# Kernel tuning notes

Hardware: AMD Instinct MI355X
Metric: run time of the kernel (lower is better)

Reference implementation:

```python
import jax, jax.numpy as jnp
import numpy as np

# task -> non-background class ids, padded with -1 to fixed width 3
NBG = np.array([[0, 1, 2], [0, 3, 4], [0, 5, 6], [0, 7, 8],
                [0, 9, -1], [0, 10, -1], [0, 11, -1]], dtype=np.int32)
NEG = -1e9      # pad logit (finite stand-in for -inf, grad-safe)
SMOOTH = 1e-5
NUM_CLASSES = 12


def setup_inputs() -> dict:
    key = jax.random.key(0)
    k1, k2, k3 = jax.random.split(key, 3)
    B, C, D, H, W = 4, 12, 32, 128, 128
    inputs = jax.random.normal(k1, (B, C, D, H, W), dtype=jnp.float32)
    task_id = jax.random.randint(k2, (B,), 0, 7, dtype=jnp.int32)
    # build targets consistent with each sample's task: labels in task_nbg[task]
    raw = jax.random.randint(k3, (B, D, H, W), 0, 3, dtype=jnp.int32)
    nbg = jnp.asarray(NBG)
    ids = nbg[task_id]                                   # [B,3]
    valid_max = jnp.where(ids[:, 2] < 0, 1, 2)           # 2-class tasks: raw in {0,1}
    raw = jnp.minimum(raw, valid_max[:, None, None, None])
    targets = jnp.take_along_axis(ids, raw.reshape(B, -1), axis=1).reshape(B, D, H, W)
    return {"inputs": inputs, "targets": targets, "task_id": task_id}


def reference(inputs, targets, task_id):
    B = inputs.shape[0]
    probs = jax.nn.softmax(inputs, axis=1)               # [B,12,D,H,W]
    nbg = jnp.asarray(NBG)
    ids = nbg[task_id]                                   # [B,3]
    mask = (ids >= 0)                                    # [B,3]
    idsc = jnp.maximum(ids, 0)
    mask5 = mask[:, :, None, None, None]
    gathered = jnp.take_along_axis(probs, idsc[:, :, None, None, None], axis=1)  # [B,3,D,H,W]
    score = jnp.where(mask5, gathered, 0.0)

    # --- remapped marginal targets: labels > 0 shifted by delta ---
    t = task_id.astype(jnp.int32)
    delta = jnp.where(t <= 4, -2 * t, -t - 4)
    tm = jnp.where(targets > 0, targets + delta[:, None, None, None], targets)   # in {0,1,2}

    # --- marginal CE: log_softmax over gathered probs (note: probs, not logits, matching torch F.cross_entropy on softmaxed inputs) ---
    logits = jnp.where(mask5, gathered, NEG)
    logp = jax.nn.log_softmax(logits, axis=1)
    nll = -jnp.take_along_axis(logp, tm[:, None], axis=1)[:, 0]                  # [B,D,H,W]
    loss_marg_ce = nll.mean(axis=(1, 2, 3)).sum() / B

    # --- marginal dice (padded classes contribute exactly 0) ---
    tgt = ((targets[:, None] == idsc[:, :, None, None, None]) & mask5).astype(probs.dtype)
    inter = jnp.sum(score * tgt, axis=(2, 3, 4))
    y_sum = jnp.sum(tgt, axis=(2, 3, 4))                 # tgt is binary: tgt*tgt == tgt
    z_sum = jnp.sum(score * score, axis=(2, 3, 4))
    dice = (2 * inter + SMOOTH) / (z_sum + y_sum + SMOOTH)
    loss_marg_dice = (1.0 - dice).sum() / B

    # --- exclusion: target_e = 1 - onehot(targets, 0..11), class 0 zeroed ---
    cls = jnp.arange(NUM_CLASSES, dtype=targets.dtype)[None, :, None, None, None]
    onehot = (targets[:, None] == cls).astype(probs.dtype)
    te = 1.0 - onehot
    te = te.at[:, 0].set(0.0)
    inter_e = jnp.sum(probs * te, axis=(2, 3, 4))
    y_e = jnp.sum(te, axis=(2, 3, 4))
    z_e = jnp.sum(probs * probs, axis=(2, 3, 4))
    dice_e = (2 * inter_e + SMOOTH) / (z_e + y_e + SMOOTH)
    loss_exc_dice = dice_e.sum() / B                     # inv=True: sum of dice scores

    loss_exc_ce = (jnp.log1p(probs) * te).mean(axis=(2, 3, 4)).sum() / B

    return (loss_marg_dice, loss_marg_ce, loss_exc_dice, loss_exc_ce)
```

## Files before the change

### kernel.cpp

```cpp
#include <hip/hip_runtime.h>


#define S4 131072
#define BLOCKS_PER_B 256
#define THREADS 256
#define NVOX 524288.0f
#define SMOOTH 1e-5f

#define WRED(v) { v += __shfl_down(v,32); v += __shfl_down(v,16); \
                  v += __shfl_down(v,8);  v += __shfl_down(v,4);  \
                  v += __shfl_down(v,2);  v += __shfl_down(v,1); }

#define PROC(COMP) do {                                                        \
  float xv[12];                                                                \
  _Pragma("unroll")                                                            \
  for (int c = 0; c < 12; ++c) xv[c] = x[c].COMP;                              \
  const int tgt = tg.COMP;                                                     \
  float m = xv[0];                                                             \
  _Pragma("unroll")                                                            \
  for (int c = 1; c < 12; ++c) m = fmaxf(m, xv[c]);                            \
  float e[12]; float es = 0.f;                                                 \
  _Pragma("unroll")                                                            \
  for (int c = 0; c < 12; ++c) { e[c] = __expf(xv[c] - m); es += e[c]; }       \
  const float r = __builtin_amdgcn_rcpf(es);                                   \
  float p[12];                                                                 \
  _Pragma("unroll")                                                            \
  for (int c = 0; c < 12; ++c) {                                               \
    p[c] = e[c] * r;                                                           \
    aZ[c] += p[c] * p[c];                                                      \
    aP[c] += p[c];                                                             \
  }                                                                            \
  float slog = 0.f;                                                            \
  _Pragma("unroll")                                                            \
  for (int c = 1; c < 12; ++c) slog += __logf(1.f + p[c]);                     \
  const float g0 = p[0];                                                       \
  float g1 = 0.f, g2 = 0.f;                                                    \
  _Pragma("unroll")                                                            \
  for (int c = 1; c < 12; ++c) {                                               \
    if (c==1||c==3||c==5||c==7||c==9||c==10||c==11) g1 = (id1==c) ? p[c] : g1; \
    else                                            g2 = (id2==c) ? p[c] : g2; \
  }                                                                            \
  const bool t0 = (tgt == 0);                                                  \
  const bool t1 = (tgt == id1);                                                \
  const bool t2 = v2 && (tgt == id2);                                          \
  c0 += t0 ? 1.f : 0.f;  c1 += t1 ? 1.f : 0.f;  c2 += t2 ? 1.f : 0.f;          \
  p0S += t0 ? g0 : 0.f;  p1S += t1 ? g1 : 0.f;  p2S += t2 ? g2 : 0.f;          \
  const float pt = t1 ? g1 : (t2 ? g2 : 0.f);                                  \
  cesE += slog - __logf(1.f + pt);                                             \
  float m3 = fmaxf(g0, g1);                                                    \
  if (v2) m3 = fmaxf(m3, g2);                                                  \
  float s3 = __expf(g0 - m3) + __expf(g1 - m3);                                \
  if (v2) s3 += __expf(g2 - m3);                                               \
  const float lse = m3 + __logf(s3);                                           \
  const float gt = t0 ? g0 : (t1 ? g1 : g2);                                   \
  ces += lse - gt;                                                             \
} while (0)

__global__ void zero_acc(float* __restrict__ acc) {
  acc[threadIdx.x] = 0.f;
}

__global__ __launch_bounds__(THREADS, 4)
void marg_main(const float4* __restrict__ inp, const int4* __restrict__ tgtp,
               const int* __restrict__ task_id, float* __restrict__ acc) {
  const int b   = blockIdx.x / BLOCKS_PER_B;
  const int blk = blockIdx.x % BLOCKS_PER_B;
  const int t   = task_id[b];
  const int id1 = (t <= 4) ? 2*t + 1 : t + 5;
  const int id2 = (t <= 3) ? 2*t + 2 : -1;
  const bool v2 = (id2 >= 0);

  const float4* inB = inp  + (size_t)b * 12 * S4;
  const int4*   tgB = tgtp + (size_t)b * S4;

  float aZ[12], aP[12];
  #pragma unroll
  for (int c = 0; c < 12; ++c) { aZ[c]=0.f; aP[c]=0.f; }
  float ces=0.f, cesE=0.f, c0=0.f, c1=0.f, c2=0.f, p0S=0.f, p1S=0.f, p2S=0.f;

  #pragma unroll 1
  for (int it = 0; it < 2; ++it) {
    const int s = (blk * 2 + it) * THREADS + (int)threadIdx.x;
    float4 x[12];
    #pragma unroll
    for (int c = 0; c < 12; ++c) x[c] = inB[c * S4 + s];
    const int4 tg = tgB[s];
    PROC(x); PROC(y); PROC(z); PROC(w);
  }

  WRED(ces); WRED(cesE); WRED(c0); WRED(c1); WRED(c2);
  WRED(p0S); WRED(p1S); WRED(p2S);
  #pragma unroll
  for (int c = 0; c < 12; ++c) { WRED(aZ[c]); WRED(aP[c]); }

  __shared__ float red[4][32];
  const int lane = threadIdx.x & 63;
  const int wv   = threadIdx.x >> 6;
  if (lane == 0) {
    float* rw = red[wv];
    rw[0]=ces; rw[1]=cesE; rw[2]=c0; rw[3]=c1; rw[4]=c2;
    rw[5]=p0S; rw[6]=p1S; rw[7]=p2S;
    #pragma unroll
    for (int c = 0; c < 12; ++c) { rw[8+c]=aZ[c]; rw[20+c]=aP[c]; }
  }
  __syncthreads();
  if (threadIdx.x < 32) {
    const float sv = red[0][threadIdx.x] + red[1][threadIdx.x]
                   + red[2][threadIdx.x] + red[3][threadIdx.x];
    atomicAdd(acc + b * 64 + threadIdx.x, sv);
  }
}

__global__ void finalize(const float* __restrict__ acc,
                         const int* __restrict__ task_id,
                         float* __restrict__ out) {
  if (threadIdx.x != 0) return;
  float lmd = 0.f, lmce = 0.f, led = 0.f, lece = 0.f;
  for (int b = 0; b < 4; ++b) {
    const float* a = acc + b * 64;
    const int t   = task_id[b];
    const int id1 = (t <= 4) ? 2*t + 1 : t + 5;
    const int id2 = (t <= 3) ? 2*t + 2 : -1;

    lmce += a[0] / NVOX;
    lece += a[1] / NVOX;

    const float d0 = (2.f*a[5] + SMOOTH) / (a[8 + 0]   + a[2] + SMOOTH);
    const float d1 = (2.f*a[6] + SMOOTH) / (a[8 + id1] + a[3] + SMOOTH);
    float d2 = 1.f;
    if (id2 >= 0)
      d2 = (2.f*a[7] + SMOOTH) / (a[8 + id2] + a[4] + SMOOTH);
    lmd += (1.f - d0) + (1.f - d1) + (1.f - d2);

    led += SMOOTH / (a[8] + SMOOTH);
    for (int c = 1; c < 12; ++c) {
      const float ptc  = (c == id1) ? a[6] : ((c == id2) ? a[7] : 0.f);
      const float cntc = (c == id1) ? a[3] : ((c == id2) ? a[4] : 0.f);
      const float inter = a[20 + c] - ptc;
      const float ye    = NVOX - cntc;
      led += (2.f*inter + SMOOTH) / (a[8 + c] + ye + SMOOTH);
    }
  }
  out[0] = lmd  * 0.25f;
  out[1] = lmce * 0.25f;
  out[2] = led  * 0.25f;
  out[3] = lece * 0.25f;
}

extern "C" void kernel_launch(void* const* d_in, const int* in_sizes, int n_in,
                              void* d_out, int out_size, void* d_ws, size_t ws_size,
                              hipStream_t stream) {
  const float* inputs  = (const float*)d_in[0];
  const int*   targets = (const int*)d_in[1];
  const int*   task_id = (const int*)d_in[2];
  float* out = (float*)d_out;
  float* acc = (float*)d_ws;

  zero_acc<<<1, 256, 0, stream>>>(acc);
  marg_main<<<dim3(4 * BLOCKS_PER_B), THREADS, 0, stream>>>(
      (const float4*)inputs, (const int4*)targets, task_id, acc);
  finalize<<<1, 64, 0, stream>>>(acc, task_id, out);
}
```

Measured before the change: 167.2 us.

## Cut transcendental count and restructure reduction via shared-memory transpose

Drops the max-subtraction from the softmax and uses raw exp2 hardware builtins. The eleven log1p calls become a single log of a running product, and the 3-way log-sum-exp loses its max shift because the gathered probabilities are bounded. The per-value wave shuffle reductions are replaced by a transposed shared-memory sum. Atomics are spread onto separate cache lines, and the c0 count is derived from the other counts. This reduces transcendental and shuffle work, but it risks exp overflow on large logits and drifts from the reference's numerically stable formulation.

```diff
diff --git a/kernel.cpp b/kernel.cpp
--- a/kernel.cpp
+++ b/kernel.cpp
@@ -6,58 +6,25 @@
 #define THREADS 256
 #define NVOX 524288.0f
 #define SMOOTH 1e-5f
-
-#define WRED(v) { v += __shfl_down(v,32); v += __shfl_down(v,16); \
-                  v += __shfl_down(v,8);  v += __shfl_down(v,4);  \
-                  v += __shfl_down(v,2);  v += __shfl_down(v,1); }
-
-#define PROC(COMP) do {                                                        \
-  float xv[12];                                                                \
-  _Pragma("unroll")                                                            \
-  for (int c = 0; c < 12; ++c) xv[c] = x[c].COMP;                              \
-  const int tgt = tg.COMP;                                                     \
-  float m = xv[0];                                                             \
-  _Pragma("unroll")                                                            \
-  for (int c = 1; c < 12; ++c) m = fmaxf(m, xv[c]);                            \
-  float e[12]; float es = 0.f;                                                 \
-  _Pragma("unroll")                                                            \
-  for (int c = 0; c < 12; ++c) { e[c] = __expf(xv[c] - m); es += e[c]; }       \
-  const float r = __builtin_amdgcn_rcpf(es);                                   \
-  float p[12];                                                                 \
-  _Pragma("unroll")                                                            \
-  for (int c = 0; c < 12; ++c) {                                               \
-    p[c] = e[c] * r;                                                           \
-    aZ[c] += p[c] * p[c];                                                      \
-    aP[c] += p[c];                                                             \
-  }                                                                            \
-  float slog = 0.f;                                                            \
-  _Pragma("unroll")                                                            \
-  for (int c = 1; c < 12; ++c) slog += __logf(1.f + p[c]);                     \
-  const float g0 = p[0];                                                       \
-  float g1 = 0.f, g2 = 0.f;                                                    \
-  _Pragma("unroll")                                                            \
-  for (int c = 1; c < 12; ++c) {                                               \
-    if (c==1||c==3||c==5||c==7||c==9||c==10||c==11) g1 = (id1==c) ? p[c] : g1; \
-    else                                            g2 = (id2==c) ? p[c] : g2; \
-  }                                                                            \
-  const bool t0 = (tgt == 0);                                                  \
-  const bool t1 = (tgt == id1);                                                \
-  const bool t2 = v2 && (tgt == id2);                                          \
-  c0 += t0 ? 1.f : 0.f;  c1 += t1 ? 1.f : 0.f;  c2 += t2 ? 1.f : 0.f;          \
-  p0S += t0 ? g0 : 0.f;  p1S += t1 ? g1 : 0.f;  p2S += t2 ? g2 : 0.f;          \
-  const float pt = t1 ? g1 : (t2 ? g2 : 0.f);                                  \
-  cesE += slog - __logf(1.f + pt);                                             \
-  float m3 = fmaxf(g0, g1);                                                    \
-  if (v2) m3 = fmaxf(m3, g2);                                                  \
-  float s3 = __expf(g0 - m3) + __expf(g1 - m3);                                \
-  if (v2) s3 += __expf(g2 - m3);                                               \
-  const float lse = m3 + __logf(s3);                                           \
-  const float gt = t0 ? g0 : (t1 ? g1 : g2);                                   \
-  ces += lse - gt;                                                             \
-} while (0)
+#define L2E 1.4426950408889634f
+#define LN2 0.6931471805599453f
 
 __global__ void zero_acc(float* __restrict__ acc) {
-  acc[threadIdx.x] = 0.f;
+  acc[blockIdx.x * 256 + threadIdx.x] = 0.f;
+}
+
+#define TAIL(CM) {                                                             \
+  const int tv = tg.CM;                                                        \
+  const bool t0 = (tv == 0), t1 = (tv == id1), t2 = (tv == id2);               \
+  c1f += t1 ? 1.f : 0.f;  c2f += t2 ? 1.f : 0.f;                               \
+  p0S += t0 ? g0.CM : 0.f; p1S += t1 ? g1.CM : 0.f; p2S += t2 ? g2.CM : 0.f;   \
+  const float pt = t1 ? g1.CM : (t2 ? g2.CM : 0.f);                            \
+  cesE2 += __builtin_amdgcn_logf(prod.CM * __builtin_amdgcn_rcpf(1.f + pt));   \
+  const float s3 = __builtin_amdgcn_exp2f(g0.CM * L2E)                         \
+                 + __builtin_amdgcn_exp2f(g1.CM * L2E)                         \
+                 + __builtin_amdgcn_exp2f(g2.CM * L2E);                        \
+  const float gt = t0 ? g0.CM : (t1 ? g1.CM : g2.CM);                          \
+  ces2 += __builtin_amdgcn_logf(s3) - gt * L2E;                               \
 }
 
 __global__ __launch_bounds__(THREADS, 4)
@@ -75,40 +42,90 @@
 
   float aZ[12], aP[12];
   #pragma unroll
-  for (int c = 0; c < 12; ++c) { aZ[c]=0.f; aP[c]=0.f; }
-  float ces=0.f, cesE=0.f, c0=0.f, c1=0.f, c2=0.f, p0S=0.f, p1S=0.f, p2S=0.f;
+  for (int c = 0; c < 12; ++c) { aZ[c] = 0.f; aP[c] = 0.f; }
+  float ces2=0.f, cesE2=0.f, c1f=0.f, c2f=0.f, p0S=0.f, p1S=0.f, p2S=0.f;
 
   #pragma unroll 1
   for (int it = 0; it < 2; ++it) {
     const int s = (blk * 2 + it) * THREADS + (int)threadIdx.x;
-    float4 x[12];
+    float4 e[12];
     #pragma unroll
-    for (int c = 0; c < 12; ++c) x[c] = inB[c * S4 + s];
+    for (int c = 0; c < 12; ++c) e[c] = inB[c * S4 + s];
     const int4 tg = tgB[s];
-    PROC(x); PROC(y); PROC(z); PROC(w);
+
+    #pragma unroll
+    for (int c = 0; c < 12; ++c) {
+      e[c].x = __builtin_amdgcn_exp2f(e[c].x * L2E);
+      e[c].y = __builtin_amdgcn_exp2f(e[c].y * L2E);
+      e[c].z = __builtin_amdgcn_exp2f(e[c].z * L2E);
+      e[c].w = __builtin_amdgcn_exp2f(e[c].w * L2E);
+    }
+    float4 es = e[0];
+    #pragma unroll
+    for (int c = 1; c < 12; ++c) {
+      es.x += e[c].x; es.y += e[c].y; es.z += e[c].z; es.w += e[c].w;
+    }
+    float4 r;
+    r.x = __builtin_amdgcn_rcpf(es.x); r.y = __builtin_amdgcn_rcpf(es.y);
+    r.z = __builtin_amdgcn_rcpf(es.z); r.w = __builtin_amdgcn_rcpf(es.w);
+
+    float4 prod = make_float4(1.f, 1.f, 1.f, 1.f);
+    #pragma unroll
+    for (int c = 0; c < 12; ++c) {
+      float4 p;
+      p.x = e[c].x * r.x; p.y = e[c].y * r.y;
+      p.z = e[c].z * r.z; p.w = e[c].w * r.w;
+      aZ[c] += (p.x*p.x + p.y*p.y) + (p.z*p.z + p.w*p.w);
+      aP[c] += (p.x + p.y) + (p.z + p.w);
+      if (c > 0) {
+        prod.x = fmaf(prod.x, p.x, prod.x);
+        prod.y = fmaf(prod.y, p.y, prod.y);
+        prod.z = fmaf(prod.z, p.z, prod.z);
+        prod.w = fmaf(prod.w, p.w, prod.w);
+      }
+    }
+
+    float4 ge1, ge2;
+    switch (id1) {
+      case 1:  ge1 = e[1];  break;  case 3:  ge1 = e[3];  break;
+      case 5:  ge1 = e[5];  break;  case 7:  ge1 = e[7];  break;
+      case 9:  ge1 = e[9];  break;  case 10: ge1 = e[10]; break;
+      default: ge1 = e[11]; break;
+    }
+    switch (id2) {
+      case 2:  ge2 = e[2];  break;  case 4:  ge2 = e[4];  break;
+      case 6:  ge2 = e[6];  break;  case 8:  ge2 = e[8];  break;
+      default: ge2 = make_float4(0.f, 0.f, 0.f, 0.f); break;
+    }
+    float4 g0, g1, g2;
+    g0.x = e[0].x * r.x; g0.y = e[0].y * r.y; g0.z = e[0].z * r.z; g0.w = e[0].w * r.w;
+    g1.x = ge1.x * r.x;  g1.y = ge1.y * r.y;  g1.z = ge1.z * r.z;  g1.w = ge1.w * r.w;
+    g2.x = v2 ? ge2.x * r.x : -1e30f;  g2.y = v2 ? ge2.y * r.y : -1e30f;
+    g2.z = v2 ? ge2.z * r.z : -1e30f;  g2.w = v2 ? ge2.w * r.w : -1e30f;
+
+    TAIL(x); TAIL(y); TAIL(z); TAIL(w);
   }
 
-  WRED(ces); WRED(cesE); WRED(c0); WRED(c1); WRED(c2);
-  WRED(p0S); WRED(p1S); WRED(p2S);
+  float vals[32];
   #pragma unroll
-  for (int c = 0; c < 12; ++c) { WRED(aZ[c]); WRED(aP[c]); }
+  for (int c = 0; c < 12; ++c) { vals[c] = aZ[c]; vals[12 + c] = aP[c]; }
+  vals[24] = ces2; vals[25] = cesE2; vals[26] = c1f; vals[27] = c2f;
+  vals[28] = p0S;  vals[29] = p1S;   vals[30] = p2S; vals[31] = 0.f;
 
-  __shared__ float red[4][32];
-  const int lane = threadIdx.x & 63;
-  const int wv   = threadIdx.x >> 6;
-  if (lane == 0) {
-    float* rw = red[wv];
-    rw[0]=ces; rw[1]=cesE; rw[2]=c0; rw[3]=c1; rw[4]=c2;
-    rw[5]=p0S; rw[6]=p1S; rw[7]=p2S;
-    #pragma unroll
-    for (int c = 0; c < 12; ++c) { rw[8+c]=aZ[c]; rw[20+c]=aP[c]; }
-  }
+  __shared__ float red[32][257];
+  #pragma unroll
+  for (int v = 0; v < 32; ++v) red[v][threadIdx.x] = vals[v];
   __syncthreads();
-  if (threadIdx.x < 32) {
-    const float sv = red[0][threadIdx.x] + red[1][threadIdx.x]
-                   + red[2][threadIdx.x] + red[3][threadIdx.x];
-    atomicAdd(acc + b * 64 + threadIdx.x, sv);
-  }
+
+  const int val = threadIdx.x & 31;
+  const int seg = threadIdx.x >> 5;
+  const float* row = red[val];
+  float ssum = 0.f;
+  #pragma unroll
+  for (int k = 0; k < 32; ++k) ssum += row[seg * 32 + k];
+  ssum += __shfl_down(ssum, 32);
+  if ((threadIdx.x & 63) < 32)
+    atomicAdd(acc + (((b * 32 + val)) << 4), ssum);
 }
 
 __global__ void finalize(const float* __restrict__ acc,
@@ -117,29 +134,32 @@
   if (threadIdx.x != 0) return;
   float lmd = 0.f, lmce = 0.f, led = 0.f, lece = 0.f;
   for (int b = 0; b < 4; ++b) {
-    const float* a = acc + b * 64;
     const int t   = task_id[b];
     const int id1 = (t <= 4) ? 2*t + 1 : t + 5;
     const int id2 = (t <= 3) ? 2*t + 2 : -1;
+    #define A(v) acc[((b * 32 + (v))) << 4]
 
-    lmce += a[0] / NVOX;
-    lece += a[1] / NVOX;
+    lmce += A(24) * LN2 / NVOX;
+    lece += A(25) * LN2 / NVOX;
 
-    const float d0 = (2.f*a[5] + SMOOTH) / (a[8 + 0]   + a[2] + SMOOTH);
-    const float d1 = (2.f*a[6] + SMOOTH) / (a[8 + id1] + a[3] + SMOOTH);
+    const float c1 = A(26), c2 = A(27);
+    const float y0 = NVOX - c1 - c2;
+    const float d0 = (2.f*A(28) + SMOOTH) / (A(0)   + y0 + SMOOTH);
+    const float d1 = (2.f*A(29) + SMOOTH) / (A(id1) + c1 + SMOOTH);
     float d2 = 1.f;
     if (id2 >= 0)
-      d2 = (2.f*a[7] + SMOOTH) / (a[8 + id2] + a[4] + SMOOTH);
+      d2 = (2.f*A(30) + SMOOTH) / (A(id2) + c2 + SMOOTH);
     lmd += (1.f - d0) + (1.f - d1) + (1.f - d2);
 
-    led += SMOOTH / (a[8] + SMOOTH);
+    led += SMOOTH / (A(0) + SMOOTH);
     for (int c = 1; c < 12; ++c) {
-      const float ptc  = (c == id1) ? a[6] : ((c == id2) ? a[7] : 0.f);
-      const float cntc = (c == id1) ? a[3] : ((c == id2) ? a[4] : 0.f);
-      const float inter = a[20 + c] - ptc;
+      const float ptc  = (c == id1) ? A(29) : ((c == id2) ? A(30) : 0.f);
+      const float cntc = (c == id1) ? c1    : ((c == id2) ? c2    : 0.f);
+      const float inter = A(12 + c) - ptc;
       const float ye    = NVOX - cntc;
-      led += (2.f*inter + SMOOTH) / (a[8 + c] + ye + SMOOTH);
+      led += (2.f*inter + SMOOTH) / (A(c) + ye + SMOOTH);
     }
+    #undef A
   }
   out[0] = lmd  * 0.25f;
   out[1] = lmce * 0.25f;
@@ -156,7 +176,7 @@
   float* out = (float*)d_out;
   float* acc = (float*)d_ws;
 
-  zero_acc<<<1, 256, 0, stream>>>(acc);
+  zero_acc<<<dim3(8), 256, 0, stream>>>(acc);
   marg_main<<<dim3(4 * BLOCKS_PER_B), THREADS, 0, stream>>>(
       (const float4*)inputs, (const int4*)targets, task_id, acc);
   finalize<<<1, 64, 0, stream>>>(acc, task_id, out);
```

Result: slower. 199.1 us (+19.1%).
